# Kernel tuning notes

Measured on AMD Instinct MI355X. Metric: run time of the kernel, lower is better.

Reference implementation:

```python
import jax, jax.numpy as jnp
import numpy as np

D = 1024
NH = 16
DH = D // NH
B = 2
N = 2048
EPS = 1e-5


def setup_inputs() -> dict:
    key = jax.random.key(0)
    ks = jax.random.split(key, 12)
    s = 0.02
    return {
        "x": jax.random.normal(ks[0], (B, N, D), jnp.float32),
        "Wq": jax.random.normal(ks[1], (D, D), jnp.float32) * s,
        "Wk": jax.random.normal(ks[2], (D, D), jnp.float32) * s,
        "Wv": jax.random.normal(ks[3], (D, D), jnp.float32) * s,
        "Wo": jax.random.normal(ks[4], (D, D), jnp.float32) * s,
        "bo": jnp.zeros((D,), jnp.float32),
        "ln1_scale": jnp.ones((D,), jnp.float32),
        "ln1_shift": jnp.zeros((D,), jnp.float32),
        "ln2_scale": jnp.ones((D,), jnp.float32),
        "ln2_shift": jnp.zeros((D,), jnp.float32),
        "W1": jax.random.normal(ks[5], (4 * D, D), jnp.float32) * s,
        "b1": jnp.zeros((4 * D,), jnp.float32),
        "W2": jax.random.normal(ks[6], (D, 4 * D), jnp.float32) * s,
        "b2": jnp.zeros((D,), jnp.float32),
    }


def _layernorm(x, scale, shift):
    mean = jnp.mean(x, axis=-1, keepdims=True)
    var = jnp.mean(jnp.square(x - mean), axis=-1, keepdims=True)  # unbiased=False
    return scale * ((x - mean) / jnp.sqrt(var + EPS)) + shift


def _gelu(x):
    c = jnp.sqrt(jnp.asarray(2.0 / jnp.pi, x.dtype))
    return 0.5 * x * (1.0 + jnp.tanh(c * (x + 0.044715 * x * x * x)))


def reference(x, Wq, Wk, Wv, Wo, bo, ln1_scale, ln1_shift, ln2_scale, ln2_shift, W1, b1, W2, b2):
    Bx, Nx, d = x.shape
    # pre-MHA LN
    h = _layernorm(x, ln1_scale, ln1_shift)
    # projections (torch Linear: y = h @ W.T), no bias for Wq/Wk/Wv
    q = (h @ Wq.T).reshape(Bx, Nx, NH, DH).transpose(0, 2, 1, 3)  # [B,nh,N,dh]
    k = (h @ Wk.T).reshape(Bx, Nx, NH, DH).transpose(0, 2, 1, 3)
    v = (h @ Wv.T).reshape(Bx, Nx, NH, DH).transpose(0, 2, 1, 3)
    s = jnp.einsum("bhnd,bhmd->bhnm", q, k)  # [B,nh,N,N]
    causal = jnp.tril(jnp.ones((Nx, Nx), bool))
    s = jnp.where(causal, s, -jnp.inf)
    p = jax.nn.softmax(s / jnp.sqrt(jnp.asarray(DH, s.dtype)), axis=-1)
    pv = jnp.einsum("bhnm,bhmd->bhnd", p, v)
    pv = pv.transpose(0, 2, 1, 3).reshape(Bx, Nx, d)
    attn = pv @ Wo.T + bo
    x = x + attn  # residual (dropout is identity, dpo=0)
    # pre-FFN LN + FFN
    h = _layernorm(x, ln2_scale, ln2_shift)
    h = _gelu(h @ W1.T + b1)
    h = h @ W2.T + b2
    return x + h
```

## Files before the change

### kernel.cpp

```cpp
#include <hip/hip_runtime.h>
#include <hip/hip_bf16.h>
#include <math.h>

#define Dmod   1024
#define NHmod  16
#define DHmod  64
#define Bmod   2
#define Nmod   2048
#define Mrows  (Bmod * Nmod)
#define FF     (4 * Dmod)
#define EPSLN  1e-5f

typedef __attribute__((ext_vector_type(8))) short bf16x8;
typedef __attribute__((ext_vector_type(4))) float f32x4;
typedef unsigned short ushort_t;
typedef unsigned int uint_t;

#define MFMA16x16x32(a, b, c) __builtin_amdgcn_mfma_f32_16x16x32_bf16((a), (b), (c), 0, 0, 0)

#define AS1 __attribute__((address_space(1)))
#define AS3 __attribute__((address_space(3)))

__device__ __forceinline__ void gload_lds16(const ushort_t* g, ushort_t* l) {
    __builtin_amdgcn_global_load_lds((const AS1 uint_t*)(const void*)g,
                                     (AS3 uint_t*)(void*)l, 16, 0, 0);
}

__device__ __forceinline__ ushort_t f2bf(float f) {
    union { float f; uint_t u; } v; v.f = f;
    uint_t r = v.u + 0x7FFFu + ((v.u >> 16) & 1u);
    return (ushort_t)(r >> 16);
}

__device__ __forceinline__ float bf2f(uint_t u) {
    union { float f; uint_t u; } v; v.u = u << 16;
    return v.f;
}

__global__ __launch_bounds__(256) void cvt_kernel(const float* __restrict__ Wq, const float* __restrict__ Wk,
                                                  const float* __restrict__ Wv, const float* __restrict__ Wo,
                                                  const float* __restrict__ W1, const float* __restrict__ W2,
                                                  ushort_t* __restrict__ qkv, ushort_t* __restrict__ wo,
                                                  ushort_t* __restrict__ w1, ushort_t* __restrict__ w2) {
    int u = blockIdx.x * 256 + threadIdx.x;
    const float* src; ushort_t* dst; int i;
    float scale = 1.0f;
    if (u < 393216) {
        if (u < 131072)      { src = Wq; dst = qkv;           i = u; scale = 0.125f; }
        else if (u < 262144) { src = Wk; dst = qkv + 1048576; i = u - 131072; }
        else                 { src = Wv; dst = qkv + 2097152; i = u - 262144; }
    } else if (u < 524288)   { src = Wo; dst = wo; i = u - 393216; }
    else if (u < 1048576)    { src = W1; dst = w1; i = u - 524288; }
    else                     { src = W2; dst = w2; i = u - 1048576; }
    float4 a = ((const float4*)src)[2 * i];
    float4 b = ((const float4*)src)[2 * i + 1];
    uint4 o;
    o.x = (uint_t)f2bf(a.x * scale) | ((uint_t)f2bf(a.y * scale) << 16);
    o.y = (uint_t)f2bf(a.z * scale) | ((uint_t)f2bf(a.w * scale) << 16);
    o.z = (uint_t)f2bf(b.x * scale) | ((uint_t)f2bf(b.y * scale) << 16);
    o.w = (uint_t)f2bf(b.z * scale) | ((uint_t)f2bf(b.w * scale) << 16);
    ((uint4*)dst)[i] = o;
}

__global__ __launch_bounds__(256) void ln_bf_kernel(const float* __restrict__ x,
                                                    const float* __restrict__ scale,
                                                    const float* __restrict__ shift,
                                                    ushort_t* __restrict__ out) {
    int row = blockIdx.x;
    const float4* xr = (const float4*)(x + (size_t)row * Dmod);
    float4 v = xr[threadIdx.x];
    float s  = v.x + v.y + v.z + v.w;
    float s2 = v.x*v.x + v.y*v.y + v.z*v.z + v.w*v.w;

    __shared__ float rs[8], rs2[8];
    #pragma unroll
    for (int o = 32; o; o >>= 1) { s += __shfl_down(s, o); s2 += __shfl_down(s2, o); }
    int wave = threadIdx.x >> 6, lane = threadIdx.x & 63;
    if (lane == 0) { rs[wave] = s; rs2[wave] = s2; }
    __syncthreads();
    if (threadIdx.x == 0) {
        rs[0]  = rs[0] + rs[1] + rs[2] + rs[3];
        rs2[0] = rs2[0] + rs2[1] + rs2[2] + rs2[3];
    }
    __syncthreads();
    float mean = rs[0] * (1.0f / Dmod);
    float var  = rs2[0] * (1.0f / Dmod) - mean * mean;
    float rstd = rsqrtf(var + EPSLN);

    float4 sc = ((const float4*)scale)[threadIdx.x];
    float4 sh = ((const float4*)shift)[threadIdx.x];
    uint2 o;
    o.x = (uint_t)f2bf(sc.x * (v.x - mean) * rstd + sh.x) |
          ((uint_t)f2bf(sc.y * (v.y - mean) * rstd + sh.y) << 16);
    o.y = (uint_t)f2bf(sc.z * (v.z - mean) * rstd + sh.z) |
          ((uint_t)f2bf(sc.w * (v.w - mean) * rstd + sh.w) << 16);
    ((uint2*)(out + (size_t)row * Dmod))[threadIdx.x] = o;
}

__device__ __forceinline__ float gelu_f(float x) {
    const float c = 0.7978845608028654f;
    float u = c * (x + 0.044715f * x * x * x);
    return x / (1.0f + __expf(-2.0f * u));
}

#define DSR(D, A, OFF) asm volatile("ds_read_b128 %0, %1 offset:" OFF : "=v"(D) : "v"(A))
#define SB0 __builtin_amdgcn_sched_barrier(0)
#define BARR __builtin_amdgcn_s_barrier()
#define LGKM(N) asm volatile("s_waitcnt lgkmcnt(" #N ")" ::)

#define GRP_QM0(J, B) \
  acc[0][J]=MFMA16x16x32(a0,B,acc[0][J]); acc[1][J]=MFMA16x16x32(a1,B,acc[1][J]); \
  acc[2][J]=MFMA16x16x32(a2,B,acc[2][J]); acc[3][J]=MFMA16x16x32(a3,B,acc[3][J]);
#define GRP_QM1(I, A) \
  acc[I][0]=MFMA16x16x32(A,b0,acc[I][0]); acc[I][1]=MFMA16x16x32(A,b1,acc[I][1]); \
  acc[I][2]=MFMA16x16x32(A,b2,acc[I][2]); acc[I][3]=MFMA16x16x32(A,b3,acc[I][3]);

template <int MODE>
__global__ __launch_bounds__(512, 2) void gemm256(const ushort_t* __restrict__ A,
                                                  const ushort_t* __restrict__ W,
                                                  const float* __restrict__ bias,
                                                  void* __restrict__ Cv,
                                                  int M, int Nout, int K, int KS,
                                                  int GN, int GM) {
    __shared__ ushort_t Ab[32768];
    __shared__ ushort_t Bb[32768];
    int tid = threadIdx.x;
    int w  = tid >> 6, l = tid & 63;
    int li = l & 15,  g = l >> 4;
    int wm = w >> 2,  wn = w & 3;

    int xcd = blockIdx.x & 7;
    int c   = blockIdx.x >> 3;
    int RN = GN >> 2, RM = GM >> 1;
    int rsz = RN * RM;
    int bz = c / rsz;
    int r  = c - bz * rsz;
    int bm = (xcd >> 2) * RM + r / RN;
    int bn = (xcd & 3) * RN + r % RN;

    int lc   = (l & 7) ^ (l >> 3);
    int sgr  = w * 32 + 2 * (l >> 3) + (lc >> 2);
    int colo = (lc & 3) * 8;
    const ushort_t* sA0 = A + (size_t)(bm * 256 + sgr) * K + bz * KS + colo;
    const ushort_t* sA1 = sA0 + (size_t)16 * K;
    const ushort_t* sB0 = W + (size_t)(bn * 256 + sgr) * K + bz * KS + colo;
    const ushort_t* sB1 = sB0 + (size_t)16 * K;

    uint_t chunkpos = (uint_t)(((((li & 1) << 2) + g) ^ (li >> 1)) << 4);
    uint_t aBase = (uint_t)(uintptr_t)(&Ab[0]) + (uint_t)(wm * 8192 + (li >> 1) * 128) + chunkpos;
    uint_t bBase = (uint_t)(uintptr_t)(&Bb[0]) + (uint_t)(wn * 4096 + (li >> 1) * 128) + chunkpos;

    f32x4 acc[8][4];
    #pragma unroll
    for (int i = 0; i < 8; i++)
        #pragma unroll
        for (int j = 0; j < 4; j++) acc[i][j] = (f32x4){0.f, 0.f, 0.f, 0.f};

    const int NT = KS >> 6;

    auto stage_all = [&](int dst, int t) {
        int kn = t * 64;
        ushort_t* dA = &Ab[0] + dst * 16384 + w * 1024;
        ushort_t* dB = &Bb[0] + dst * 16384 + w * 1024;
        gload_lds16(sA0 + kn,      dA);        gload_lds16(sA1 + kn,      dA + 512);
        gload_lds16(sB0 + kn,      dB);        gload_lds16(sB1 + kn,      dB + 512);
        gload_lds16(sA0 + kn + 32, dA + 8192); gload_lds16(sA1 + kn + 32, dA + 8192 + 512);
        gload_lds16(sB0 + kn + 32, dB + 8192); gload_lds16(sB1 + kn + 32, dB + 8192 + 512);
    };

    stage_all(0, 0);
    asm volatile("s_waitcnt vmcnt(0)" ::);
    SB0; BARR;

    for (int t = 0; t < NT; ++t) {
        int d = t & 1;
        uint_t aAddr = aBase + (uint_t)(d * 32768);
        uint_t bAddr = bBase + (uint_t)(d * 32768);
        bf16x8 a0, a1, a2, a3, b0, b1, b2, b3;

        DSR(a0, aAddr, "0");    DSR(a1, aAddr, "1024");
        DSR(a2, aAddr, "2048"); DSR(a3, aAddr, "3072");
        DSR(b0, bAddr, "0");    DSR(b1, bAddr, "1024");
        DSR(b2, bAddr, "2048"); DSR(b3, bAddr, "3072");
        if (t + 1 < NT) stage_all(d ^ 1, t + 1);
        SB0;
        LGKM(3); SB0;
        __builtin_amdgcn_s_setprio(1);
        GRP_QM0(0, b0)
        LGKM(2); SB0;
        GRP_QM0(1, b1)
        LGKM(1); SB0;
        GRP_QM0(2, b2)
        LGKM(0); SB0;
        GRP_QM0(3, b3)
        __builtin_amdgcn_s_setprio(0);

        DSR(a0, aAddr, "4096"); DSR(a1, aAddr, "5120");
        DSR(a2, aAddr, "6144"); DSR(a3, aAddr, "7168");
        SB0;
        LGKM(3); SB0;
        __builtin_amdgcn_s_setprio(1);
        GRP_QM1(4, a0)
        LGKM(2); SB0;
        GRP_QM1(5, a1)
        LGKM(1); SB0;
        GRP_QM1(6, a2)
        LGKM(0); SB0;
        GRP_QM1(7, a3)
        __builtin_amdgcn_s_setprio(0);

        DSR(a0, aAddr, "16384"); DSR(a1, aAddr, "17408");
        DSR(a2, aAddr, "18432"); DSR(a3, aAddr, "19456");
        DSR(b0, bAddr, "16384"); DSR(b1, bAddr, "17408");
        DSR(b2, bAddr, "18432"); DSR(b3, bAddr, "19456");
        SB0;
        LGKM(3); SB0;
        __builtin_amdgcn_s_setprio(1);
        GRP_QM0(0, b0)
        LGKM(2); SB0;
        GRP_QM0(1, b1)
        LGKM(1); SB0;
        GRP_QM0(2, b2)
        LGKM(0); SB0;
        GRP_QM0(3, b3)
        __builtin_amdgcn_s_setprio(0);

        DSR(a0, aAddr, "20480"); DSR(a1, aAddr, "21504");
        DSR(a2, aAddr, "22528"); DSR(a3, aAddr, "23552");
        SB0;
        LGKM(3); SB0;
        __builtin_amdgcn_s_setprio(1);
        GRP_QM1(4, a0)
        LGKM(2); SB0;
        GRP_QM1(5, a1)
        LGKM(1); SB0;
        GRP_QM1(6, a2)
        LGKM(0); SB0;
        GRP_QM1(7, a3)
        __builtin_amdgcn_s_setprio(0);

        asm volatile("s_waitcnt vmcnt(0)" ::);
        SB0; BARR;
    }

    #pragma unroll
    for (int fm = 0; fm < 8; fm++) {
        #pragma unroll
        for (int fn = 0; fn < 4; fn++) {
            int nn = bn * 256 + wn * 64 + fn * 16 + li;
            int mB = bm * 256 + wm * 128 + (fm >> 2) * 64 + (fm & 3) * 16 + g * 4;
            if (MODE == 0) {
                int which = nn >> 10, col = nn & 1023;
                int h = col >> 6, dd = col & 63;
                int b = mB >> 11, n0 = mB & (Nmod - 1);
                ushort_t* C = (ushort_t*)Cv;
                if (which == 2) {
                    uint2 pk;
                    pk.x = (uint_t)f2bf(acc[fm][fn][0]) | ((uint_t)f2bf(acc[fm][fn][1]) << 16);
                    pk.y = (uint_t)f2bf(acc[fm][fn][2]) | ((uint_t)f2bf(acc[fm][fn][3]) << 16);
                    *(uint2*)(C + 8388608u + (((size_t)(b * NHmod + h)) * DHmod + dd) * Nmod + n0) = pk;
                } else {
                    #pragma unroll
                    for (int r2 = 0; r2 < 4; r2++) {
                        size_t idx = (size_t)which * 4194304u +
                                     (((size_t)(b * NHmod + h)) * Nmod + n0 + r2) * DHmod + dd;
                        C[idx] = f2bf(acc[fm][fn][r2]);
                    }
                }
            } else if (MODE == 2) {
                ushort_t* C = (ushort_t*)Cv;
                #pragma unroll
                for (int r2 = 0; r2 < 4; r2++)
                    C[(size_t)(mB + r2) * Nout + nn] = f2bf(gelu_f(acc[fm][fn][r2] + bias[nn]));
            } else {
                ushort_t* P = (ushort_t*)Cv + (size_t)bz * M * Nout;
                #pragma unroll
                for (int r2 = 0; r2 < 4; r2++)
                    P[(size_t)(mB + r2) * Nout + nn] = f2bf(acc[fm][fn][r2]);
            }
        }
    }
}

__global__ __launch_bounds__(256) void red_ln4_kernel(const ushort_t* __restrict__ p,
                                                      const float* __restrict__ x,
                                                      const float* __restrict__ bo,
                                                      const float* __restrict__ scale,
                                                      const float* __restrict__ shift,
                                                      float* __restrict__ x1,
                                                      ushort_t* __restrict__ h2) {
    int row = blockIdx.x;
    int t   = threadIdx.x;
    const size_t MD = (size_t)Mrows * Dmod;
    size_t i = (size_t)row * 256 + t;
    float4 xr = ((const float4*)(x + (size_t)row * Dmod))[t];
    float4 bb = ((const float4*)bo)[t];
    float4 v;
    v.x = xr.x + bb.x; v.y = xr.y + bb.y; v.z = xr.z + bb.z; v.w = xr.w + bb.w;
    #pragma unroll
    for (int z = 0; z < 4; z++) {
        uint2 pk = ((const uint2*)(p + (size_t)z * MD))[i];
        v.x += bf2f(pk.x & 0xffffu);
        v.y += bf2f(pk.x >> 16);
        v.z += bf2f(pk.y & 0xffffu);
        v.w += bf2f(pk.y >> 16);
    }
    ((float4*)(x1 + (size_t)row * Dmod))[t] = v;

    float s  = v.x + v.y + v.z + v.w;
    float s2 = v.x*v.x + v.y*v.y + v.z*v.z + v.w*v.w;
    __shared__ float rs[8], rs2[8];
    #pragma unroll
    for (int o = 32; o; o >>= 1) { s += __shfl_down(s, o); s2 += __shfl_down(s2, o); }
    int wave = t >> 6, lane = t & 63;
    if (lane == 0) { rs[wave] = s; rs2[wave] = s2; }
    __syncthreads();
    if (t == 0) {
        rs[0]  = rs[0] + rs[1] + rs[2] + rs[3];
        rs2[0] = rs2[0] + rs2[1] + rs2[2] + rs2[3];
    }
    __syncthreads();
    float mean = rs[0] * (1.0f / Dmod);
    float var  = rs2[0] * (1.0f / Dmod) - mean * mean;
    float rstd = rsqrtf(var + EPSLN);

    float4 sc = ((const float4*)scale)[t];
    float4 sh = ((const float4*)shift)[t];
    uint2 o;
    o.x = (uint_t)f2bf(sc.x * (v.x - mean) * rstd + sh.x) |
          ((uint_t)f2bf(sc.y * (v.y - mean) * rstd + sh.y) << 16);
    o.y = (uint_t)f2bf(sc.z * (v.z - mean) * rstd + sh.z) |
          ((uint_t)f2bf(sc.w * (v.w - mean) * rstd + sh.w) << 16);
    ((uint2*)(h2 + (size_t)row * Dmod))[t] = o;
}

__global__ __launch_bounds__(256) void red_out4_kernel(const ushort_t* __restrict__ p,
                                                       const float* __restrict__ x1,
                                                       const float* __restrict__ b2,
                                                       float* __restrict__ out) {
    const size_t MD4 = (size_t)Mrows * Dmod / 4;
    size_t i = (size_t)blockIdx.x * 256 + threadIdx.x;
    if (i >= MD4) return;
    float4 xr = ((const float4*)x1)[i];
    float4 bb = ((const float4*)b2)[i & 255];
    float4 v;
    v.x = xr.x + bb.x; v.y = xr.y + bb.y; v.z = xr.z + bb.z; v.w = xr.w + bb.w;
    #pragma unroll
    for (int z = 0; z < 4; z++) {
        uint2 pk = ((const uint2*)(p + (size_t)z * Mrows * Dmod))[i];
        v.x += bf2f(pk.x & 0xffffu);
        v.y += bf2f(pk.x >> 16);
        v.z += bf2f(pk.y & 0xffffu);
        v.w += bf2f(pk.y >> 16);
    }
    ((float4*)out)[i] = v;
}

__global__ __launch_bounds__(256) void fattn_kernel(const ushort_t* __restrict__ Q,
                                                    const ushort_t* __restrict__ K,
                                                    const ushort_t* __restrict__ VT,
                                                    ushort_t* __restrict__ O) {
    int bid = blockIdx.x;
    int xcd = bid & 7;
    int j   = bid >> 3;
    int bh  = xcd * 4 + (j & 3);
    int qt  = 31 - (j >> 2);
    int b   = bh >> 4, hh = bh & 15;
    int w    = threadIdx.x >> 6;
    int lane = threadIdx.x & 63;
    int li   = lane & 15;
    int g    = lane >> 4;

    __shared__ ushort_t Klds[2][4096];
    __shared__ ushort_t Vlds[2][4096];
    __shared__ ushort_t Plds[4][16][72];

    int q0 = qt * 64 + w * 16;
    int q  = q0 + li;

    const ushort_t* Qb = Q  + (size_t)bh * Nmod * DHmod;
    const ushort_t* Kb = K  + (size_t)bh * Nmod * DHmod;
    const ushort_t* Vb = VT + (size_t)bh * DHmod * Nmod;

    bf16x8 qf[2];
    #pragma unroll
    for (int c = 0; c < 2; c++)
        qf[c] = *(const bf16x8*)(Qb + (size_t)q * DHmod + c * 32 + g * 8);

    f32x4 po[4];
    #pragma unroll
    for (int mt = 0; mt < 4; mt++) po[mt] = (f32x4){0.f, 0.f, 0.f, 0.f};
    float l = 0.f;

    const int ntiles = qt + 1;

    int r_sub = lane >> 3;
    int cc    = ((lane & 7) ^ (r_sub & 7)) * 8;

    int swz  = (li & 7) * 8;
    int roff = li * 64;
    int c0k  = (g * 8) ^ swz;
    int c1k  = (32 + g * 8) ^ swz;

    auto stage = [&](int buf, int kt) {
        int k0 = kt * 64;
        #pragma unroll
        for (int i2 = 0; i2 < 2; i2++) {
            int i   = w * 2 + i2;
            int row = i * 8 + r_sub;
            gload_lds16(Kb + (size_t)(k0 + row) * DHmod + cc, &Klds[buf][i * 512]);
            gload_lds16(Vb + (size_t)row * Nmod + k0 + cc,    &Vlds[buf][i * 512]);
        }
    };

    stage(0, 0);

    for (int kt = 0; kt < ntiles; ++kt) {
        __syncthreads();
        if (kt + 1 < ntiles) stage((kt + 1) & 1, kt + 1);
        int cur = kt & 1;
        int k0  = kt * 64;

        f32x4 s[4];
        __builtin_amdgcn_s_setprio(1);
        #pragma unroll
        for (int mt = 0; mt < 4; mt++) {
            bf16x8 kf0 = *(const bf16x8*)&Klds[cur][mt * 1024 + roff + c0k];
            bf16x8 kf1 = *(const bf16x8*)&Klds[cur][mt * 1024 + roff + c1k];
            s[mt] = (f32x4){0.f, 0.f, 0.f, 0.f};
            s[mt] = MFMA16x16x32(kf0, qf[0], s[mt]);
            s[mt] = MFMA16x16x32(kf1, qf[1], s[mt]);
        }
        __builtin_amdgcn_s_setprio(0);

        if (kt == qt) {
            #pragma unroll
            for (int mt = 0; mt < 4; mt++)
                #pragma unroll
                for (int r = 0; r < 4; r++)
                    if (k0 + mt * 16 + g * 4 + r > q) s[mt][r] = -INFINITY;
        }
        float ptile = 0.f;
        #pragma unroll
        for (int mt = 0; mt < 4; mt++) {
            float p0 = __expf(s[mt][0]);
            float p1 = __expf(s[mt][1]);
            float p2 = __expf(s[mt][2]);
            float p3 = __expf(s[mt][3]);
            ptile += (p0 + p1) + (p2 + p3);
            uint2 pk;
            pk.x = (uint_t)f2bf(p0) | ((uint_t)f2bf(p1) << 16);
            pk.y = (uint_t)f2bf(p2) | ((uint_t)f2bf(p3) << 16);
            *(uint2*)&Plds[w][li][mt * 16 + g * 4] = pk;
        }
        l += ptile;

        asm volatile("" ::: "memory");

        bf16x8 pf0 = *(const bf16x8*)&Plds[w][li][g * 8];
        bf16x8 pf1 = *(const bf16x8*)&Plds[w][li][32 + g * 8];
        __builtin_amdgcn_s_setprio(1);
        #pragma unroll
        for (int mt = 0; mt < 4; mt++) {
            bf16x8 vf0 = *(const bf16x8*)&Vlds[cur][mt * 1024 + roff + c0k];
            bf16x8 vf1 = *(const bf16x8*)&Vlds[cur][mt * 1024 + roff + c1k];
            po[mt] = MFMA16x16x32(vf0, pf0, po[mt]);
            po[mt] = MFMA16x16x32(vf1, pf1, po[mt]);
        }
        __builtin_amdgcn_s_setprio(0);
        asm volatile("" ::: "memory");
    }

    l += __shfl_xor(l, 16);
    l += __shfl_xor(l, 32);
    float inv = 1.0f / l;
    ushort_t* Orow = O + ((size_t)(b * Nmod + q)) * Dmod + hh * DHmod;
    #pragma unroll
    for (int mt = 0; mt < 4; mt++) {
        uint2 pk;
        pk.x = (uint_t)f2bf(po[mt][0] * inv) | ((uint_t)f2bf(po[mt][1] * inv) << 16);
        pk.y = (uint_t)f2bf(po[mt][2] * inv) | ((uint_t)f2bf(po[mt][3] * inv) << 16);
        *(uint2*)(Orow + mt * 16 + g * 4) = pk;
    }
}

extern "C" void kernel_launch(void* const* d_in, const int* in_sizes, int n_in,
                              void* d_out, int out_size, void* d_ws, size_t ws_size,
                              hipStream_t stream) {
    const float* x    = (const float*)d_in[0];
    const float* Wq   = (const float*)d_in[1];
    const float* Wk   = (const float*)d_in[2];
    const float* Wv   = (const float*)d_in[3];
    const float* Wo   = (const float*)d_in[4];
    const float* bo   = (const float*)d_in[5];
    const float* ln1s = (const float*)d_in[6];
    const float* ln1b = (const float*)d_in[7];
    const float* ln2s = (const float*)d_in[8];
    const float* ln2b = (const float*)d_in[9];
    const float* W1   = (const float*)d_in[10];
    const float* b1   = (const float*)d_in[11];
    const float* W2   = (const float*)d_in[12];
    const float* b2   = (const float*)d_in[13];
    float* out = (float*)d_out;
    char*  wsb = (char*)d_ws;

    ushort_t* h_bf  = (ushort_t*)wsb;
    ushort_t* qb    = (ushort_t*)(wsb + (8u  << 20));
    ushort_t* kb    = qb + 4194304;
    ushort_t* vtb   = qb + 8388608;
    float*    x1    = (float*)(wsb + (32u << 20));
    ushort_t* h2_bf = (ushort_t*)(wsb + (48u << 20));
    ushort_t* g_bf  = (ushort_t*)(wsb + (56u << 20));
    ushort_t* wqkv  = (ushort_t*)(wsb + (88u << 20));
    ushort_t* wo_b  = (ushort_t*)(wsb + (94u << 20));
    ushort_t* w1_b  = (ushort_t*)(wsb + (96u << 20));
    ushort_t* w2_b  = (ushort_t*)(wsb + (104u << 20));
    ushort_t* att   = h_bf;
    ushort_t* pWoB = (ushort_t*)(wsb + (56u << 20));
    ushort_t* pFd  = (ushort_t*)wsb;

    cvt_kernel<<<6144, 256, 0, stream>>>(Wq, Wk, Wv, Wo, W1, W2, wqkv, wo_b, w1_b, w2_b);
    ln_bf_kernel<<<Mrows, 256, 0, stream>>>(x, ln1s, ln1b, h_bf);
    gemm256<0><<<192, 512, 0, stream>>>(h_bf, wqkv, nullptr, qb, Mrows, 3072, Dmod, Dmod, 12, 16);
    fattn_kernel<<<1024, 256, 0, stream>>>(qb, kb, vtb, att);
    gemm256<4><<<256, 512, 0, stream>>>(att, wo_b, nullptr, pWoB, Mrows, Dmod, Dmod, Dmod / 4, 4, 16);
    red_ln4_kernel<<<Mrows, 256, 0, stream>>>(pWoB, x, bo, ln2s, ln2b, x1, h2_bf);
    gemm256<2><<<256, 512, 0, stream>>>(h2_bf, w1_b, b1, g_bf, Mrows, FF, Dmod, Dmod, 16, 16);
    gemm256<4><<<256, 512, 0, stream>>>(g_bf, w2_b, nullptr, pFd, Mrows, Dmod, FF, FF / 4, 4, 16);
    red_out4_kernel<<<(Mrows * Dmod / 4 + 255) / 256, 256, 0, stream>>>(pFd, x1, b2, out);
}
```

Measured before the change: 219.4 us.

## Load GEMM A operand directly from global into registers, bypassing LDS

The A tile no longer goes through LDS. Each wave issues global_load_dwordx4 straight into MFMA operand registers for its 128 rows, and software-pipelines the next k-tile's loads after each MFMA group using fine-grained vmcnt waits. Only the B tile stays double-buffered in LDS. This halves LDS footprint and ds_read traffic, but raises register pressure and depends on uncoalesced global reads being served from cache, along with hand-tuned vmcnt counts that are fragile.

```diff
diff --git a/kernel.cpp b/kernel.cpp
--- a/kernel.cpp
+++ b/kernel.cpp
@@ -107,13 +107,15 @@
 #define SB0 __builtin_amdgcn_sched_barrier(0)
 #define BARR __builtin_amdgcn_s_barrier()
 #define LGKM(N) asm volatile("s_waitcnt lgkmcnt(" #N ")" ::)
-
-#define GRP_QM0(J, B) \
-  acc[0][J]=MFMA16x16x32(a0,B,acc[0][J]); acc[1][J]=MFMA16x16x32(a1,B,acc[1][J]); \
-  acc[2][J]=MFMA16x16x32(a2,B,acc[2][J]); acc[3][J]=MFMA16x16x32(a3,B,acc[3][J]);
-#define GRP_QM1(I, A) \
-  acc[I][0]=MFMA16x16x32(A,b0,acc[I][0]); acc[I][1]=MFMA16x16x32(A,b1,acc[I][1]); \
-  acc[I][2]=MFMA16x16x32(A,b2,acc[I][2]); acc[I][3]=MFMA16x16x32(A,b3,acc[I][3]);
+#define VMC(N) asm volatile("s_waitcnt vmcnt(" #N ")" ::)
+#define ALOAD(D, P) asm volatile("global_load_dwordx4 %0, %1, off" : "=v"(D) : "v"(P))
+
+#define GJA(J, B, A0, A1, A2, A3) \
+  acc[0][J]=MFMA16x16x32(A0,B,acc[0][J]); acc[1][J]=MFMA16x16x32(A1,B,acc[1][J]); \
+  acc[2][J]=MFMA16x16x32(A2,B,acc[2][J]); acc[3][J]=MFMA16x16x32(A3,B,acc[3][J]);
+#define GJB(J, B, A0, A1, A2, A3) \
+  acc[4][J]=MFMA16x16x32(A0,B,acc[4][J]); acc[5][J]=MFMA16x16x32(A1,B,acc[5][J]); \
+  acc[6][J]=MFMA16x16x32(A2,B,acc[6][J]); acc[7][J]=MFMA16x16x32(A3,B,acc[7][J]);
 
 template <int MODE>
 __global__ __launch_bounds__(512, 2) void gemm256(const ushort_t* __restrict__ A,
@@ -122,7 +124,6 @@
                                                   void* __restrict__ Cv,
                                                   int M, int Nout, int K, int KS,
                                                   int GN, int GM) {
-    __shared__ ushort_t Ab[32768];
     __shared__ ushort_t Bb[32768];
     int tid = threadIdx.x;
     int w  = tid >> 6, l = tid & 63;
@@ -141,14 +142,22 @@
     int lc   = (l & 7) ^ (l >> 3);
     int sgr  = w * 32 + 2 * (l >> 3) + (lc >> 2);
     int colo = (lc & 3) * 8;
-    const ushort_t* sA0 = A + (size_t)(bm * 256 + sgr) * K + bz * KS + colo;
-    const ushort_t* sA1 = sA0 + (size_t)16 * K;
     const ushort_t* sB0 = W + (size_t)(bn * 256 + sgr) * K + bz * KS + colo;
     const ushort_t* sB1 = sB0 + (size_t)16 * K;
 
     uint_t chunkpos = (uint_t)(((((li & 1) << 2) + g) ^ (li >> 1)) << 4);
-    uint_t aBase = (uint_t)(uintptr_t)(&Ab[0]) + (uint_t)(wm * 8192 + (li >> 1) * 128) + chunkpos;
     uint_t bBase = (uint_t)(uintptr_t)(&Bb[0]) + (uint_t)(wn * 4096 + (li >> 1) * 128) + chunkpos;
+
+    const ushort_t* Abase = A + (size_t)(bm * 256 + wm * 128 + li) * K + bz * KS + g * 8;
+    const size_t K16 = (size_t)16 * K;
+    const ushort_t* pR0 = Abase;
+    const ushort_t* pR1 = pR0 + K16;
+    const ushort_t* pR2 = pR1 + K16;
+    const ushort_t* pR3 = pR2 + K16;
+    const ushort_t* pR4 = pR3 + K16;
+    const ushort_t* pR5 = pR4 + K16;
+    const ushort_t* pR6 = pR5 + K16;
+    const ushort_t* pR7 = pR6 + K16;
 
     f32x4 acc[8][4];
     #pragma unroll
@@ -158,88 +167,91 @@
 
     const int NT = KS >> 6;
 
-    auto stage_all = [&](int dst, int t) {
-        int kn = t * 64;
-        ushort_t* dA = &Ab[0] + dst * 16384 + w * 1024;
-        ushort_t* dB = &Bb[0] + dst * 16384 + w * 1024;
-        gload_lds16(sA0 + kn,      dA);        gload_lds16(sA1 + kn,      dA + 512);
-        gload_lds16(sB0 + kn,      dB);        gload_lds16(sB1 + kn,      dB + 512);
-        gload_lds16(sA0 + kn + 32, dA + 8192); gload_lds16(sA1 + kn + 32, dA + 8192 + 512);
-        gload_lds16(sB0 + kn + 32, dB + 8192); gload_lds16(sB1 + kn + 32, dB + 8192 + 512);
-    };
-
-    stage_all(0, 0);
-    asm volatile("s_waitcnt vmcnt(0)" ::);
+    bf16x8 af0, af1, af2, af3, af4, af5, af6, af7;
+    bf16x8 af8, af9, af10, af11, af12, af13, af14, af15;
+    bf16x8 b0, b1, b2, b3;
+
+    {
+        ushort_t* dB = (ushort_t*)&Bb[0] + w * 1024;
+        gload_lds16(sB0,      dB);        gload_lds16(sB1,      dB + 512);
+        gload_lds16(sB0 + 32, dB + 8192); gload_lds16(sB1 + 32, dB + 8192 + 512);
+        ALOAD(af0,  pR0); ALOAD(af1,  pR1); ALOAD(af2,  pR2); ALOAD(af3,  pR3);
+        ALOAD(af4,  pR4); ALOAD(af5,  pR5); ALOAD(af6,  pR6); ALOAD(af7,  pR7);
+        ALOAD(af8,  pR0 + 32); ALOAD(af9,  pR1 + 32); ALOAD(af10, pR2 + 32); ALOAD(af11, pR3 + 32);
+        ALOAD(af12, pR4 + 32); ALOAD(af13, pR5 + 32); ALOAD(af14, pR6 + 32); ALOAD(af15, pR7 + 32);
+    }
+    VMC(12);
     SB0; BARR;
 
     for (int t = 0; t < NT; ++t) {
         int d = t & 1;
-        uint_t aAddr = aBase + (uint_t)(d * 32768);
+        bool pf = (t + 1 < NT);
         uint_t bAddr = bBase + (uint_t)(d * 32768);
-        bf16x8 a0, a1, a2, a3, b0, b1, b2, b3;
-
-        DSR(a0, aAddr, "0");    DSR(a1, aAddr, "1024");
-        DSR(a2, aAddr, "2048"); DSR(a3, aAddr, "3072");
+        int kn0 = (t + 1) * 64;
+        int kn1 = kn0 + 32;
+
         DSR(b0, bAddr, "0");    DSR(b1, bAddr, "1024");
         DSR(b2, bAddr, "2048"); DSR(b3, bAddr, "3072");
-        if (t + 1 < NT) stage_all(d ^ 1, t + 1);
+        if (pf) {
+            ushort_t* dB = (ushort_t*)&Bb[0] + (d ^ 1) * 16384 + w * 1024;
+            gload_lds16(sB0 + kn0,      dB);        gload_lds16(sB1 + kn0,      dB + 512);
+            gload_lds16(sB0 + kn0 + 32, dB + 8192); gload_lds16(sB1 + kn0 + 32, dB + 8192 + 512);
+        }
         SB0;
         LGKM(3); SB0;
         __builtin_amdgcn_s_setprio(1);
-        GRP_QM0(0, b0)
+        GJA(0, b0, af0, af1, af2, af3)
         LGKM(2); SB0;
-        GRP_QM0(1, b1)
+        GJA(1, b1, af0, af1, af2, af3)
         LGKM(1); SB0;
-        GRP_QM0(2, b2)
+        GJA(2, b2, af0, af1, af2, af3)
         LGKM(0); SB0;
-        GRP_QM0(3, b3)
+        GJA(3, b3, af0, af1, af2, af3)
         __builtin_amdgcn_s_setprio(0);
-
-        DSR(a0, aAddr, "4096"); DSR(a1, aAddr, "5120");
-        DSR(a2, aAddr, "6144"); DSR(a3, aAddr, "7168");
+        if (pf) { ALOAD(af0, pR0 + kn0); ALOAD(af1, pR1 + kn0); ALOAD(af2, pR2 + kn0); ALOAD(af3, pR3 + kn0); }
+        SB0;
+
+        if (pf) { VMC(16); } else { VMC(8); }
+        SB0;
+        __builtin_amdgcn_s_setprio(1);
+        GJB(0, b0, af4, af5, af6, af7)
+        GJB(1, b1, af4, af5, af6, af7)
+        GJB(2, b2, af4, af5, af6, af7)
+        GJB(3, b3, af4, af5, af6, af7)
+        __builtin_amdgcn_s_setprio(0);
+        if (pf) { ALOAD(af4, pR4 + kn0); ALOAD(af5, pR5 + kn0); ALOAD(af6, pR6 + kn0); ALOAD(af7, pR7 + kn0); }
+        SB0;
+
+        DSR(b0, bAddr, "16384"); DSR(b1, bAddr, "17408");
+        DSR(b2, bAddr, "18432"); DSR(b3, bAddr, "19456");
+        SB0;
+        if (pf) { VMC(16); } else { VMC(4); }
         SB0;
         LGKM(3); SB0;
         __builtin_amdgcn_s_setprio(1);
-        GRP_QM1(4, a0)
+        GJA(0, b0, af8, af9, af10, af11)
         LGKM(2); SB0;
-        GRP_QM1(5, a1)
+        GJA(1, b1, af8, af9, af10, af11)
         LGKM(1); SB0;
-        GRP_QM1(6, a2)
+        GJA(2, b2, af8, af9, af10, af11)
         LGKM(0); SB0;
-        GRP_QM1(7, a3)
+        GJA(3, b3, af8, af9, af10, af11)
         __builtin_amdgcn_s_setprio(0);
-
-        DSR(a0, aAddr, "16384"); DSR(a1, aAddr, "17408");
-        DSR(a2, aAddr, "18432"); DSR(a3, aAddr, "19456");
-        DSR(b0, bAddr, "16384"); DSR(b1, bAddr, "17408");
-        DSR(b2, bAddr, "18432"); DSR(b3, bAddr, "19456");
-        SB0;
-        LGKM(3); SB0;
+        if (pf) { ALOAD(af8, pR0 + kn1); ALOAD(af9, pR1 + kn1); ALOAD(af10, pR2 + kn1); ALOAD(af11, pR3 + kn1); }
+        SB0;
+
+        if (pf) { VMC(16); } else { VMC(0); }
+        SB0;
         __builtin_amdgcn_s_setprio(1);
-        GRP_QM0(0, b0)
-        LGKM(2); SB0;
-        GRP_QM0(1, b1)
-        LGKM(1); SB0;
-        GRP_QM0(2, b2)
-        LGKM(0); SB0;
-        GRP_QM0(3, b3)
+        GJB(0, b0, af12, af13, af14, af15)
+        GJB(1, b1, af12, af13, af14, af15)
+        GJB(2, b2, af12, af13, af14, af15)
+        GJB(3, b3, af12, af13, af14, af15)
         __builtin_amdgcn_s_setprio(0);
-
-        DSR(a0, aAddr, "20480"); DSR(a1, aAddr, "21504");
-        DSR(a2, aAddr, "22528"); DSR(a3, aAddr, "23552");
-        SB0;
-        LGKM(3); SB0;
-        __builtin_amdgcn_s_setprio(1);
-        GRP_QM1(4, a0)
-        LGKM(2); SB0;
-        GRP_QM1(5, a1)
-        LGKM(1); SB0;
-        GRP_QM1(6, a2)
-        LGKM(0); SB0;
-        GRP_QM1(7, a3)
-        __builtin_amdgcn_s_setprio(0);
-
-        asm volatile("s_waitcnt vmcnt(0)" ::);
+        if (pf) { ALOAD(af12, pR4 + kn1); ALOAD(af13, pR5 + kn1); ALOAD(af14, pR6 + kn1); ALOAD(af15, pR7 + kn1); }
+        SB0;
+
+        if (pf) { VMC(12); }
         SB0; BARR;
     }
 
```

After: 332.5 us. 51.5% more time.
